# Kernel optimization log

Measured on AMD Instinct MI355X. Metric: run time of the kernel, lower is better.

## Reference

```python
import jax, jax.numpy as jnp
import numpy as np

# Model dims
D_MODEL = 768
N_LAYER = 2
VOCAB = 32000
D_STATE = 16
D_INNER = 2 * D_MODEL          # expand=2
DT_RANK = D_MODEL // 16        # 48
D_CONV = 4
EPS = 1e-5


def rmsnorm(x, w):
    return x * jax.lax.rsqrt(jnp.mean(x * x, axis=-1, keepdims=True) + EPS) * w


def selective_scan(u, delta, A, B, C, D):
    # u: (b,l,di) delta: (b,l,di) A: (di,n) B,C: (b,l,n) D: (di,)
    def step(h, inp):
        delta_t, B_t, C_t, u_t = inp  # (b,di),(b,n),(b,n),(b,di)
        dA = jnp.exp(delta_t[..., None] * A)                      # (b,di,n)
        dBu = delta_t[..., None] * B_t[:, None, :] * u_t[..., None]
        h = dA * h + dBu
        y = jnp.einsum('bdn,bn->bd', h, C_t)
        return h, y

    b = u.shape[0]
    h0 = jnp.zeros((b, D_INNER, D_STATE), dtype=u.dtype)
    xs = (jnp.swapaxes(delta, 0, 1), jnp.swapaxes(B, 0, 1),
          jnp.swapaxes(C, 0, 1), jnp.swapaxes(u, 0, 1))
    _, ys = jax.lax.scan(step, h0, xs)        # ys: (l,b,di)
    y = jnp.swapaxes(ys, 0, 1)
    return y + u * D


def mamba_block(x, in_proj_w, conv_w, conv_b, x_proj_w, dt_proj_w, dt_proj_b,
                A_log, D, out_proj_w):
    b, l, d = x.shape
    xr = x @ in_proj_w.T                       # (b,l,2*di)
    u, res = jnp.split(xr, 2, axis=-1)
    # causal depthwise conv over seq
    uc = jnp.swapaxes(u, 1, 2)                 # (b,di,l)
    uc = jax.lax.conv_general_dilated(
        uc, conv_w[:, None, :], window_strides=(1,),
        padding=[(D_CONV - 1, 0)], feature_group_count=D_INNER,
        dimension_numbers=('NCH', 'OIH', 'NCH'))
    u = jax.nn.silu(jnp.swapaxes(uc + conv_b[None, :, None], 1, 2))
    # ssm
    A = -jnp.exp(A_log)                        # (di,n)
    x_dbl = u @ x_proj_w.T                     # (b,l,dt_rank+2n)
    delta, B, C = jnp.split(x_dbl, [DT_RANK, DT_RANK + D_STATE], axis=-1)
    delta = jax.nn.softplus(delta @ dt_proj_w.T + dt_proj_b)   # (b,l,di)
    y = selective_scan(u, delta, A, B, C, D)
    y = y * jax.nn.silu(res)
    return y @ out_proj_w.T


def setup_inputs() -> dict:
    key = jax.random.key(0)
    ks = jax.random.split(key, 12)
    s = 0.02
    L = N_LAYER
    inp = {
        'input_ids': jax.random.randint(ks[0], (2, 1024), 0, VOCAB),
        'emb': jax.random.normal(ks[1], (VOCAB, D_MODEL), jnp.float32) * s,
        'norm_w': jnp.ones((L, D_MODEL), jnp.float32),
        'in_proj_w': jax.random.normal(ks[2], (L, 2 * D_INNER, D_MODEL), jnp.float32) * s,
        'conv_w': jax.random.normal(ks[3], (L, D_INNER, D_CONV), jnp.float32) * s,
        'conv_b': jnp.zeros((L, D_INNER), jnp.float32),
        'x_proj_w': jax.random.normal(ks[4], (L, DT_RANK + 2 * D_STATE, D_INNER), jnp.float32) * s,
        'dt_proj_w': jax.random.normal(ks[5], (L, D_INNER, DT_RANK), jnp.float32) * s,
        'dt_proj_b': jax.random.normal(ks[6], (L, D_INNER), jnp.float32) * s,
        'A_log': jnp.log(jnp.broadcast_to(jnp.arange(1, D_STATE + 1, dtype=jnp.float32),
                                          (L, D_INNER, D_STATE))),
        'D': jnp.ones((L, D_INNER), jnp.float32),
        'out_proj_w': jax.random.normal(ks[7], (L, D_MODEL, D_INNER), jnp.float32) * s,
        'norm_f_w': jnp.ones((D_MODEL,), jnp.float32),
    }
    return inp


def reference(input_ids, emb, norm_w, in_proj_w, conv_w, conv_b, x_proj_w,
              dt_proj_w, dt_proj_b, A_log, D, out_proj_w, norm_f_w):
    x = emb[input_ids]                         # (b,l,d)
    for i in range(N_LAYER):
        x = x + mamba_block(rmsnorm(x, norm_w[i]), in_proj_w[i], conv_w[i],
                            conv_b[i], x_proj_w[i], dt_proj_w[i], dt_proj_b[i],
                            A_log[i], D[i], out_proj_w[i])
    x = rmsnorm(x, norm_f_w)
    logits = x @ emb.T                         # tied lm_head
    return logits
```

## Files before the change

kernel.cpp:

```cpp
#include <hip/hip_runtime.h>
#include <hip/hip_bf16.h>
#include <cstdint>
#include <cstddef>

#define D_MODEL 768
#define D_INNER 1536
#define DT_RANK 48
#define D_STATE 16
#define SEQ     1024
#define BATCH   2
#define NROWS   2048
#define VOCAB   32000
#define LCHUNK  16
#define NCHUNK  64
#define CHST    49152

typedef __hip_bfloat16 bf16;
typedef short bf16x8 __attribute__((ext_vector_type(8)));
typedef float f32x4  __attribute__((ext_vector_type(4)));
struct bf8 { bf16 v[8]; };

__device__ __forceinline__ void async_copy16(void* lds, const void* gp) {
    __builtin_amdgcn_global_load_lds(
        (const __attribute__((address_space(1))) unsigned int*)gp,
        (__attribute__((address_space(3)))       unsigned int*)lds,
        16, 0, 0);
}


#define LDSP(BUF, AB) (smem + (((BUF)*2 + (AB)) << 15))

#define PHB() do { \
  __builtin_amdgcn_sched_barrier(0); \
  __builtin_amdgcn_s_barrier(); \
  __builtin_amdgcn_sched_barrier(0); \
} while (0)

#define WAIT_VMCNT(n) do { \
  asm volatile("s_waitcnt vmcnt(" #n ")" ::: "memory"); \
  __builtin_amdgcn_sched_barrier(0); \
} while (0)

#define STAGE_A(BUF, H, KT) do { \
  const int ru0_ = (H)*64 + wave*8; \
  const int ru1_ = ru0_ + 128; \
  const bf16* ga0_ = Ag + (size_t)(m0 + ru0_ + (lane >> 3)) * (size_t)K + (size_t)((KT)*64 + swz8); \
  const bf16* ga1_ = Ag + (size_t)(m0 + ru1_ + (lane >> 3)) * (size_t)K + (size_t)((KT)*64 + swz8); \
  async_copy16(LDSP(BUF, 0) + ru0_*128, ga0_); \
  async_copy16(LDSP(BUF, 0) + ru1_*128, ga1_); \
} while (0)

#define STAGE_B(BUF, H, KT) do { \
  const int lb0_ = wave*8, lb1_ = 64 + wave*8; \
  const int rb0_ = ((lb0_ >> 5) << 6) + (H)*32 + (lb0_ & 31); \
  const int rb1_ = ((lb1_ >> 5) << 6) + (H)*32 + (lb1_ & 31); \
  const bf16* gb0_ = Bg + (size_t)(n0 + rb0_ + (lane >> 3)) * (size_t)K + (size_t)((KT)*64 + swz8); \
  const bf16* gb1_ = Bg + (size_t)(n0 + rb1_ + (lane >> 3)) * (size_t)K + (size_t)((KT)*64 + swz8); \
  async_copy16(LDSP(BUF, 1) + rb0_*128, gb0_); \
  async_copy16(LDSP(BUF, 1) + rb1_*128, gb1_); \
} while (0)

#define RDA4(BUF, MH) do { \
  _Pragma("unroll") \
  for (int i2_ = 0; i2_ < 4; ++i2_) { \
    const char* rp_ = LDSP(BUF, 0) + (wr*128 + (MH)*64 + i2_*16 + fm) * 128; \
    a[i2_][0] = *(const bf16x8*)(rp_ + (((kqi    ) ^ fm7) << 4)); \
    a[i2_][1] = *(const bf16x8*)(rp_ + (((4 + kqi) ^ fm7) << 4)); \
  } \
} while (0)

#define RDB4(BUF, NH, DST) do { \
  _Pragma("unroll") \
  for (int j2_ = 0; j2_ < 2; ++j2_) { \
    const char* rp_ = LDSP(BUF, 1) + (wc*64 + (NH)*32 + j2_*16 + fm) * 128; \
    DST[j2_][0] = *(const bf16x8*)(rp_ + (((kqi    ) ^ fm7) << 4)); \
    DST[j2_][1] = *(const bf16x8*)(rp_ + (((4 + kqi) ^ fm7) << 4)); \
  } \
} while (0)

#define QMFMA(MH, NH, BB) do { \
  __builtin_amdgcn_s_setprio(1); \
  _Pragma("unroll") \
  for (int i2_ = 0; i2_ < 4; ++i2_) { \
    _Pragma("unroll") \
    for (int j2_ = 0; j2_ < 2; ++j2_) { \
      acc[(MH)*4 + i2_][(NH)*2 + j2_] = __builtin_amdgcn_mfma_f32_16x16x32_bf16( \
          a[i2_][0], BB[j2_][0], acc[(MH)*4 + i2_][(NH)*2 + j2_], 0, 0, 0); \
      acc[(MH)*4 + i2_][(NH)*2 + j2_] = __builtin_amdgcn_mfma_f32_16x16x32_bf16( \
          a[i2_][1], BB[j2_][1], acc[(MH)*4 + i2_][(NH)*2 + j2_], 0, 0, 0); \
    } \
  } \
  __builtin_amdgcn_s_setprio(0); \
} while (0)

#define ITER(TT, LAST) do { \
  RDA4(0, 0); RDB4(0, 0, b0); \
  STAGE_B(1, 1, (TT) + 1); \
  PHB(); QMFMA(0, 0, b0); PHB(); \
  RDB4(0, 1, b1); \
  if (!(LAST)) STAGE_A(0, 0, (TT) + 2); \
  PHB(); QMFMA(0, 1, b1); PHB(); \
  RDA4(0, 1); \
  if (!(LAST)) STAGE_B(0, 0, (TT) + 2); \
  PHB(); QMFMA(1, 0, b0); PHB(); \
  if (!(LAST)) { STAGE_A(0, 1, (TT) + 2); WAIT_VMCNT(6); } else { WAIT_VMCNT(0); } \
  PHB(); QMFMA(1, 1, b1); PHB(); \
  RDA4(1, 0); RDB4(1, 0, b0); \
  if (!(LAST)) STAGE_B(0, 1, (TT) + 2); \
  PHB(); QMFMA(0, 0, b0); PHB(); \
  RDB4(1, 1, b1); \
  if (!(LAST)) STAGE_A(1, 0, (TT) + 3); \
  PHB(); QMFMA(0, 1, b1); PHB(); \
  RDA4(1, 1); \
  if (!(LAST)) STAGE_B(1, 0, (TT) + 3); \
  PHB(); QMFMA(1, 0, b0); PHB(); \
  if (!(LAST)) { STAGE_A(1, 1, (TT) + 3); WAIT_VMCNT(6); } else { WAIT_VMCNT(0); } \
  PHB(); QMFMA(1, 1, b1); PHB(); \
} while (0)

__global__ __launch_bounds__(512, 2) void gemm256(
    const bf16* __restrict__ Ag, const bf16* __restrict__ Bg,
    float* __restrict__ C, int M, int N, int K, int ntm)
{
    (void)M;
    __shared__ __align__(16) char smem[131072];

    const int cpx  = gridDim.x >> 3;
    const int bid  = blockIdx.x;
    const int wgid = (bid & 7) * cpx + (bid >> 3);
    const int m0 = (wgid % ntm) << 8;
    const int n0 = (wgid / ntm) << 8;

    const int t    = threadIdx.x;
    const int wave = t >> 6, lane = t & 63;
    const int wr = wave >> 2, wc = wave & 3;
    const int fm  = lane & 15, fm7 = lane & 7;
    const int kqi = lane >> 4;
    const int swz8 = (((lane & 7) ^ ((lane >> 3) & 7)) << 3);
    const int nkt = K >> 6;

    f32x4 acc[8][4];
    #pragma unroll
    for (int i = 0; i < 8; ++i)
        #pragma unroll
        for (int j = 0; j < 4; ++j)
            acc[i][j] = {0.f, 0.f, 0.f, 0.f};

    bf16x8 a[4][2], b0[2][2], b1[2][2];

    STAGE_A(0, 0, 0); STAGE_A(0, 1, 0); STAGE_B(0, 0, 0); STAGE_B(0, 1, 0);
    WAIT_VMCNT(4);
    STAGE_A(1, 0, 1); STAGE_A(1, 1, 1); STAGE_B(1, 0, 1);
    WAIT_VMCNT(6);
    PHB();

    int tt = 0;
    #pragma unroll 1
    for (; tt + 2 < nkt; tt += 2) { ITER(tt, false); }
    ITER(tt, true);

    const int lr = (lane >> 4) * 4;
    const int lc = lane & 15;
    #pragma unroll
    for (int i = 0; i < 8; ++i) {
        #pragma unroll
        for (int j = 0; j < 4; ++j) {
            const size_t base = (size_t)(m0 + wr*128 + i*16 + lr) * N
                              + (size_t)(n0 + wc*64 + j*16 + lc);
            #pragma unroll
            for (int r = 0; r < 4; ++r)
                C[base + (size_t)r * N] = acc[i][j][r];
        }
    }
}

template<int EPI>
__global__ __launch_bounds__(256) void gemm_bt(
    const bf16* __restrict__ A, const bf16* __restrict__ B,
    float* __restrict__ C, const float* __restrict__ bias,
    int M, int N, int K, int lda, int ntm)
{
    __shared__ bf16 sA[128 * 32];
    __shared__ bf16 sB[128 * 32];
    const int bid  = blockIdx.x;
    const int m0   = (bid % ntm) * 128;
    const int n0   = (bid / ntm) * 128;
    const int koff = blockIdx.y * K;
    const int t    = threadIdx.x;
    const int wave = t >> 6;
    const int lane = t & 63;
    const int r0 = wave * 16 + (lane >> 2);
    const int c0 = (lane & 3) * 8;
    const int wm = (wave & 1) * 64;
    const int wn = (wave >> 1) * 64;
    const int fm = lane & 15;
    const int kq = (lane >> 4) * 8;

    f32x4 acc[4][4];
    #pragma unroll
    for (int i = 0; i < 4; ++i)
        #pragma unroll
        for (int j = 0; j < 4; ++j)
            acc[i][j] = {0.f, 0.f, 0.f, 0.f};

    int nr0 = n0 + r0;      if (nr0 > N - 1) nr0 = N - 1;
    int nr1 = n0 + 64 + r0; if (nr1 > N - 1) nr1 = N - 1;

    const bf16* gA0 = A + (size_t)(m0 + r0)      * lda + koff + c0;
    const bf16* gA1 = A + (size_t)(m0 + 64 + r0) * lda + koff + c0;
    const bf16* gB0 = B + (size_t)nr0 * lda + koff + c0;
    const bf16* gB1 = B + (size_t)nr1 * lda + koff + c0;
    char* lA0 = (char*)sA + wave * 1024;
    char* lA1 = (char*)sA + 4096 + wave * 1024;
    char* lB0 = (char*)sB + wave * 1024;
    char* lB1 = (char*)sB + 4096 + wave * 1024;

    C += (size_t)blockIdx.y * M * N;

    for (int k0 = 0; k0 < K; k0 += 32) {
        async_copy16(lA0, gA0 + k0);
        async_copy16(lA1, gA1 + k0);
        async_copy16(lB0, gB0 + k0);
        async_copy16(lB1, gB1 + k0);
        __syncthreads();

        bf16x8 af[4], bfr[4];
        #pragma unroll
        for (int i = 0; i < 4; ++i) {
            af[i]  = *(const bf16x8*)&sA[(wm + i * 16 + fm) * 32 + kq];
            bfr[i] = *(const bf16x8*)&sB[(wn + i * 16 + fm) * 32 + kq];
        }
        #pragma unroll
        for (int i = 0; i < 4; ++i)
            #pragma unroll
            for (int j = 0; j < 4; ++j)
                acc[i][j] = __builtin_amdgcn_mfma_f32_16x16x32_bf16(
                    af[i], bfr[j], acc[i][j], 0, 0, 0);
        __syncthreads();
    }

    const int lr = (lane >> 4) * 4;
    const int lc = lane & 15;
    #pragma unroll
    for (int i = 0; i < 4; ++i) {
        #pragma unroll
        for (int j = 0; j < 4; ++j) {
            const int col = n0 + wn + j * 16 + lc;
            if (col >= N) continue;
            #pragma unroll
            for (int r = 0; r < 4; ++r) {
                const int row = m0 + wm + i * 16 + lr + r;
                const size_t o = (size_t)row * N + col;
                float v = acc[i][j][r];
                if (EPI == 1) {
                    C[o] += v;
                } else if (EPI == 2) {
                    v += bias[col];
                    v = (v > 15.f) ? v : __logf(1.f + __expf(v));
                    C[o] = v;
                } else {
                    C[o] = v;
                }
            }
        }
    }
}

__global__ __launch_bounds__(256) void reduce4_kernel(
    const float* __restrict__ p, float* __restrict__ o, int n)
{
    const int i = blockIdx.x * 256 + threadIdx.x;
    if (i >= n) return;
    o[i] = p[i] + p[i + n] + p[i + 2 * n] + p[i + 3 * n];
}

__global__ __launch_bounds__(192) void embed_kernel(
    const int* __restrict__ ids, const float* __restrict__ emb,
    float* __restrict__ x)
{
    const int row = blockIdx.x;
    const int t = threadIdx.x;
    const float4* src = (const float4*)(emb + (size_t)ids[row] * D_MODEL);
    float4* dst = (float4*)(x + (size_t)row * D_MODEL);
    dst[t] = src[t];
}

__global__ __launch_bounds__(256) void rmsnorm_kernel(
    const float* __restrict__ x, const float* __restrict__ w,
    bf16* __restrict__ out)
{
    const int row = blockIdx.x;
    const float* xr = x + (size_t)row * D_MODEL;
    const int t = threadIdx.x;
    float v0 = xr[t], v1 = xr[t + 256], v2 = xr[t + 512];
    float s = v0 * v0 + v1 * v1 + v2 * v2;
    #pragma unroll
    for (int m = 1; m < 64; m <<= 1) s += __shfl_xor(s, m);
    __shared__ float red[4];
    if ((t & 63) == 0) red[t >> 6] = s;
    __syncthreads();
    s = red[0] + red[1] + red[2] + red[3];
    const float sc = rsqrtf(s * (1.f / 768.f) + 1e-5f);
    bf16* o = out + (size_t)row * D_MODEL;
    o[t]       = __float2bfloat16(v0 * sc * w[t]);
    o[t + 256] = __float2bfloat16(v1 * sc * w[t + 256]);
    o[t + 512] = __float2bfloat16(v2 * sc * w[t + 512]);
}

__global__ __launch_bounds__(256) void cvt_bf16_kernel(
    const float* __restrict__ src, bf16* __restrict__ dst, int n)
{
    const int i = (blockIdx.x * 256 + threadIdx.x) * 8;
    if (i >= n) return;
    const float4 a = *(const float4*)(src + i);
    const float4 b = *(const float4*)(src + i + 4);
    bf8 o;
    o.v[0] = __float2bfloat16(a.x); o.v[1] = __float2bfloat16(a.y);
    o.v[2] = __float2bfloat16(a.z); o.v[3] = __float2bfloat16(a.w);
    o.v[4] = __float2bfloat16(b.x); o.v[5] = __float2bfloat16(b.y);
    o.v[6] = __float2bfloat16(b.z); o.v[7] = __float2bfloat16(b.w);
    *(bf8*)(dst + i) = o;
}

__global__ __launch_bounds__(256) void cvt_layer_weights(
    const float* __restrict__ ipw, const float* __restrict__ xpw,
    const float* __restrict__ dtw, const float* __restrict__ opw,
    bf16* __restrict__ wip, bf16* __restrict__ wxp,
    bf16* __restrict__ wdt, bf16* __restrict__ wop)
{
    int i = blockIdx.x * 256 + threadIdx.x;
    if (i < 3072 * 768) { wip[i] = __float2bfloat16(ipw[i]); return; }
    i -= 3072 * 768;
    if (i < 80 * 1536)  { wxp[i] = __float2bfloat16(xpw[i]); return; }
    i -= 80 * 1536;
    if (i < 1536 * 64) {
        const int r = i >> 6, c = i & 63;
        wdt[i] = __float2bfloat16(c < DT_RANK ? dtw[r * DT_RANK + c] : 0.f);
        return;
    }
    i -= 1536 * 64;
    if (i < 768 * 1536) { wop[i] = __float2bfloat16(opw[i]); }
}

__global__ __launch_bounds__(256) void pad_dt_kernel(
    const float* __restrict__ x_dbl, bf16* __restrict__ out)
{
    const int i = blockIdx.x * 256 + threadIdx.x;
    const int r = i >> 6, c = i & 63;
    out[i] = __float2bfloat16(c < DT_RANK ? x_dbl[r * 80 + c] : 0.f);
}

__global__ __launch_bounds__(256) void conv_silu_kernel(
    const float* __restrict__ xr, const float* __restrict__ cw,
    const float* __restrict__ cb, float* __restrict__ uf,
    bf16* __restrict__ ub)
{
    const int idx = blockIdx.x * 256 + threadIdx.x;
    const int di  = idx % D_INNER;
    const int row = idx / D_INNER;
    const int l   = row & (SEQ - 1);
    float acc = cb[di];
    #pragma unroll
    for (int j = 0; j < 4; ++j) {
        const int ll = l - 3 + j;
        if (ll >= 0)
            acc += cw[di * 4 + j] * xr[(size_t)(row - 3 + j) * 3072 + di];
    }
    const float s = acc / (1.f + __expf(-acc));
    uf[idx] = s;
    ub[idx] = __float2bfloat16(s);
}

__global__ __launch_bounds__(256) void scan_pass1(
    const float* __restrict__ delta, const float* __restrict__ u,
    const float* __restrict__ x_dbl, const float* __restrict__ A_log,
    float* __restrict__ P, float* __restrict__ H)
{
    const int n  = threadIdx.x & 15;
    const int g  = threadIdx.x >> 4;
    const int ch = blockIdx.x * 16 + g;
    const int k  = blockIdx.y;
    const int b  = ch / D_INNER;
    const int di = ch % D_INNER;
    const int t0 = k * LCHUNK;

    const float An = -__expf(A_log[di * D_STATE + n]);
    const float* drow = delta + ((size_t)b * SEQ + t0) * D_INNER + di;
    const float* urow = u     + ((size_t)b * SEQ + t0) * D_INNER + di;
    const float* xdr  = x_dbl + ((size_t)b * SEQ + t0) * 80;

    float h = 0.f, ap = 1.f;
    #pragma unroll
    for (int t = 0; t < LCHUNK; ++t) {
        const float dv = drow[t * D_INNER];
        const float uv = urow[t * D_INNER];
        const float Bv = xdr[t * 80 + 48 + n];
        const float a  = __expf(dv * An);
        h = a * h + (dv * Bv) * uv;
        ap *= a;
    }
    const size_t o = (size_t)k * CHST + ch * 16 + n;
    P[o] = ap;
    H[o] = h;
}

__global__ __launch_bounds__(256) void scan_pass2(
    const float* __restrict__ P, const float* __restrict__ H,
    float* __restrict__ Hin)
{
    const int id = blockIdx.x * 256 + threadIdx.x;
    float h = 0.f;
    #pragma unroll 16
    for (int k = 0; k < NCHUNK; ++k) {
        const size_t o = (size_t)k * CHST + id;
        Hin[o] = h;
        h = P[o] * h + H[o];
    }
}

__global__ __launch_bounds__(256) void scan_pass3(
    const float* __restrict__ delta, const float* __restrict__ u,
    const float* __restrict__ x_dbl, const float* __restrict__ xr,
    const float* __restrict__ A_log, const float* __restrict__ Dp,
    const float* __restrict__ Hin, bf16* __restrict__ yb)
{
    const int n  = threadIdx.x & 15;
    const int g  = threadIdx.x >> 4;
    const int ch = blockIdx.x * 16 + g;
    const int k  = blockIdx.y;
    const int b  = ch / D_INNER;
    const int di = ch % D_INNER;
    const int t0 = k * LCHUNK;

    const float An = -__expf(A_log[di * D_STATE + n]);
    const float Dv = Dp[di];
    const float* drow = delta + ((size_t)b * SEQ + t0) * D_INNER + di;
    const float* urow = u     + ((size_t)b * SEQ + t0) * D_INNER + di;
    const float* rrow = xr + ((size_t)b * SEQ + t0) * 3072 + D_INNER + di;
    const float* xdr  = x_dbl + ((size_t)b * SEQ + t0) * 80;
    bf16* yrow = yb + ((size_t)b * SEQ + t0) * D_INNER + di;

    float h = Hin[(size_t)k * CHST + ch * 16 + n];
    #pragma unroll
    for (int t = 0; t < LCHUNK; ++t) {
        const float dv = drow[t * D_INNER];
        const float uv = urow[t * D_INNER];
        const float Bv = xdr[t * 80 + 48 + n];
        const float Cv = xdr[t * 80 + 64 + n];
        const float a  = __expf(dv * An);
        h = a * h + (dv * Bv) * uv;
        float p = h * Cv;
        p += __shfl_xor(p, 1);
        p += __shfl_xor(p, 2);
        p += __shfl_xor(p, 4);
        p += __shfl_xor(p, 8);
        if (n == 0) {
            float y = p + uv * Dv;
            const float r = rrow[t * 3072];
            y *= r / (1.f + __expf(-r));
            yrow[t * D_INNER] = __float2bfloat16(y);
        }
    }
}

extern "C" void kernel_launch(void* const* d_in, const int* in_sizes, int n_in,
                              void* d_out, int out_size, void* d_ws, size_t ws_size,
                              hipStream_t stream)
{
    const int*   ids    = (const int*)  d_in[0];
    const float* emb    = (const float*)d_in[1];
    const float* norm_w = (const float*)d_in[2];
    const float* ipw    = (const float*)d_in[3];
    const float* cw     = (const float*)d_in[4];
    const float* cb     = (const float*)d_in[5];
    const float* xpw    = (const float*)d_in[6];
    const float* dtw    = (const float*)d_in[7];
    const float* dtb    = (const float*)d_in[8];
    const float* alog   = (const float*)d_in[9];
    const float* Dp     = (const float*)d_in[10];
    const float* opw    = (const float*)d_in[11];
    const float* nfw    = (const float*)d_in[12];
    float* out = (float*)d_out;

    char* ws = (char*)d_ws;
    bf16*  emb_bf = (bf16*)ws;  ws += (size_t)VOCAB * D_MODEL * 2;
    float* x      = (float*)ws; ws += (size_t)NROWS * D_MODEL * 4;
    bf16*  xn     = (bf16*)ws;  ws += (size_t)NROWS * D_MODEL * 2;
    bf16*  ub     = (bf16*)ws;  ws += (size_t)NROWS * D_INNER * 2;
    float* xdbl   = (float*)ws; ws += (size_t)NROWS * 80 * 4;
    bf16*  dtraw  = (bf16*)ws;  ws += (size_t)NROWS * 64 * 2;
    bf16*  yb     = (bf16*)ws;  ws += (size_t)NROWS * D_INNER * 2;
    bf16*  wip    = (bf16*)ws;  ws += (size_t)3072 * 768 * 2;
    bf16*  wxp    = (bf16*)ws;  ws += (size_t)80 * 1536 * 2;
    bf16*  wdt    = (bf16*)ws;  ws += (size_t)1536 * 64 * 2;
    bf16*  wop    = (bf16*)ws;  ws += (size_t)768 * 1536 * 2;

    char* ob = (char*)d_out;
    float* xr    = (float*)ob;  ob += (size_t)NROWS * 3072 * 4;
    float* uf    = (float*)ob;  ob += (size_t)NROWS * D_INNER * 4;
    float* delta = (float*)ob;  ob += (size_t)NROWS * D_INNER * 4;
    float* Pbuf  = (float*)ob;  ob += (size_t)NCHUNK * CHST * 4;
    float* Hbuf  = (float*)ob;  ob += (size_t)NCHUNK * CHST * 4;
    float* Hin   = (float*)ob;  ob += (size_t)NCHUNK * CHST * 4;
    float* xpart = (float*)ob;  ob += (size_t)4 * NROWS * 80 * 4;

    cvt_bf16_kernel<<<VOCAB * D_MODEL / 8 / 256, 256, 0, stream>>>(
        emb, emb_bf, VOCAB * D_MODEL);
    embed_kernel<<<NROWS, 192, 0, stream>>>(ids, emb, x);

    for (int l = 0; l < 2; ++l) {
        cvt_layer_weights<<<(3760128 + 255) / 256, 256, 0, stream>>>(
            ipw + (size_t)l * 3072 * 768, xpw + (size_t)l * 80 * 1536,
            dtw + (size_t)l * 1536 * DT_RANK, opw + (size_t)l * 768 * 1536,
            wip, wxp, wdt, wop);
        rmsnorm_kernel<<<NROWS, 256, 0, stream>>>(x, norm_w + l * D_MODEL, xn);
        gemm_bt<0><<<16 * 24, 256, 0, stream>>>(xn, wip, xr, nullptr,
                                                NROWS, 3072, D_MODEL, D_MODEL, 16);
        conv_silu_kernel<<<NROWS * D_INNER / 256, 256, 0, stream>>>(
            xr, cw + (size_t)l * D_INNER * 4, cb + (size_t)l * D_INNER, uf, ub);
        gemm_bt<0><<<dim3(16, 4), 256, 0, stream>>>(ub, wxp, xpart, nullptr,
                                                    NROWS, 80, 384, D_INNER, 16);
        reduce4_kernel<<<(NROWS * 80 + 255) / 256, 256, 0, stream>>>(
            xpart, xdbl, NROWS * 80);
        pad_dt_kernel<<<NROWS * 64 / 256, 256, 0, stream>>>(xdbl, dtraw);
        gemm_bt<2><<<16 * 12, 256, 0, stream>>>(dtraw, wdt, delta,
                                                dtb + (size_t)l * D_INNER,
                                                NROWS, D_INNER, 64, 64, 16);
        scan_pass1<<<dim3(192, NCHUNK), 256, 0, stream>>>(
            delta, uf, xdbl, alog + (size_t)l * D_INNER * D_STATE, Pbuf, Hbuf);
        scan_pass2<<<CHST / 256, 256, 0, stream>>>(Pbuf, Hbuf, Hin);
        scan_pass3<<<dim3(192, NCHUNK), 256, 0, stream>>>(
            delta, uf, xdbl, xr, alog + (size_t)l * D_INNER * D_STATE,
            Dp + (size_t)l * D_INNER, Hin, yb);
        gemm_bt<1><<<16 * 6, 256, 0, stream>>>(yb, wop, x, nullptr,
                                               NROWS, D_MODEL, D_INNER, D_INNER, 16);
    }

    rmsnorm_kernel<<<NROWS, 256, 0, stream>>>(x, nfw, xn);
    gemm256<<<8 * 125, 512, 0, stream>>>(xn, emb_bf, out,
                                         NROWS, VOCAB, D_MODEL, 8);
}
```

Baseline: 971.4 us.

## Fuse reductions with norm, split-K out_proj, batch weight conversion, retune scan chunks

Several changes land together. The scan chunk length goes from 16 to 32, halving the chunk count, and scan_pass2 is fully unrolled. The weight conversion for both layers is done in one launch, and the pad_dt step is folded into the x_proj split-K reduction. The out_proj GEMM now uses split-K into partial buffers, followed by a kernel that reduces the partials, adds the residual and applies the next RMSNorm. The goal is to cut launch count, raise parallelism in the out_proj GEMM and shorten the chunk-carry pass, at the cost of longer sequential per-chunk loops and extra partial-buffer traffic.

```diff
diff --git a/kernel.cpp b/kernel.cpp
--- a/kernel.cpp
+++ b/kernel.cpp
@@ -11,8 +11,8 @@
 #define BATCH   2
 #define NROWS   2048
 #define VOCAB   32000
-#define LCHUNK  16
-#define NCHUNK  64
+#define LCHUNK  32
+#define NCHUNK  32
 #define CHST    49152
 
 typedef __hip_bfloat16 bf16;
@@ -266,12 +266,50 @@
     }
 }
 
-__global__ __launch_bounds__(256) void reduce4_kernel(
-    const float* __restrict__ p, float* __restrict__ o, int n)
+__global__ __launch_bounds__(256) void reduce_xp_kernel(
+    const float* __restrict__ p, float* __restrict__ xdbl,
+    bf16* __restrict__ dtraw)
 {
     const int i = blockIdx.x * 256 + threadIdx.x;
-    if (i >= n) return;
-    o[i] = p[i] + p[i + n] + p[i + 2 * n] + p[i + 3 * n];
+    const float v = p[i] + p[i + 163840] + p[i + 327680] + p[i + 491520];
+    xdbl[i] = v;
+    const int r = i / 80, c = i - r * 80;
+    if (c < 64)
+        dtraw[(r << 6) + c] = __float2bfloat16(c < DT_RANK ? v : 0.f);
+}
+
+__global__ __launch_bounds__(256) void reduce_res_norm_kernel(
+    const float* __restrict__ part, float* __restrict__ x,
+    const float* __restrict__ w, bf16* __restrict__ out)
+{
+    const int row = blockIdx.x;
+    const size_t base = (size_t)row * D_MODEL;
+    const int t = threadIdx.x;
+    float v0, v1, v2;
+    {
+        const int e0 = t, e1 = t + 256, e2 = t + 512;
+        v0 = x[base + e0] + part[base + e0] + part[base + e0 + 1572864]
+           + part[base + e0 + 3145728] + part[base + e0 + 4718592];
+        v1 = x[base + e1] + part[base + e1] + part[base + e1 + 1572864]
+           + part[base + e1 + 3145728] + part[base + e1 + 4718592];
+        v2 = x[base + e2] + part[base + e2] + part[base + e2 + 1572864]
+           + part[base + e2 + 3145728] + part[base + e2 + 4718592];
+    }
+    x[base + t]       = v0;
+    x[base + t + 256] = v1;
+    x[base + t + 512] = v2;
+    float s = v0 * v0 + v1 * v1 + v2 * v2;
+    #pragma unroll
+    for (int m = 1; m < 64; m <<= 1) s += __shfl_xor(s, m);
+    __shared__ float red[4];
+    if ((t & 63) == 0) red[t >> 6] = s;
+    __syncthreads();
+    s = red[0] + red[1] + red[2] + red[3];
+    const float sc = rsqrtf(s * (1.f / 768.f) + 1e-5f);
+    bf16* o = out + base;
+    o[t]       = __float2bfloat16(v0 * sc * w[t]);
+    o[t + 256] = __float2bfloat16(v1 * sc * w[t + 256]);
+    o[t + 512] = __float2bfloat16(v2 * sc * w[t + 512]);
 }
 
 __global__ __launch_bounds__(192) void embed_kernel(
@@ -329,25 +367,26 @@
     bf16* __restrict__ wdt, bf16* __restrict__ wop)
 {
     int i = blockIdx.x * 256 + threadIdx.x;
-    if (i < 3072 * 768) { wip[i] = __float2bfloat16(ipw[i]); return; }
+    const int l = (i >= 3760128) ? 1 : 0;
+    i -= l * 3760128;
+    if (i < 3072 * 768) {
+        wip[l * 3072 * 768 + i] = __float2bfloat16(ipw[l * 3072 * 768 + i]);
+        return;
+    }
     i -= 3072 * 768;
-    if (i < 80 * 1536)  { wxp[i] = __float2bfloat16(xpw[i]); return; }
+    if (i < 80 * 1536) {
+        wxp[l * 80 * 1536 + i] = __float2bfloat16(xpw[l * 80 * 1536 + i]);
+        return;
+    }
     i -= 80 * 1536;
     if (i < 1536 * 64) {
         const int r = i >> 6, c = i & 63;
-        wdt[i] = __float2bfloat16(c < DT_RANK ? dtw[r * DT_RANK + c] : 0.f);
+        wdt[l * 1536 * 64 + i] = __float2bfloat16(
+            c < DT_RANK ? dtw[l * 1536 * DT_RANK + r * DT_RANK + c] : 0.f);
         return;
     }
     i -= 1536 * 64;
-    if (i < 768 * 1536) { wop[i] = __float2bfloat16(opw[i]); }
-}
-
-__global__ __launch_bounds__(256) void pad_dt_kernel(
-    const float* __restrict__ x_dbl, bf16* __restrict__ out)
-{
-    const int i = blockIdx.x * 256 + threadIdx.x;
-    const int r = i >> 6, c = i & 63;
-    out[i] = __float2bfloat16(c < DT_RANK ? x_dbl[r * 80 + c] : 0.f);
+    wop[l * 768 * 1536 + i] = __float2bfloat16(opw[l * 768 * 1536 + i]);
 }
 
 __global__ __launch_bounds__(256) void conv_silu_kernel(
@@ -410,7 +449,7 @@
 {
     const int id = blockIdx.x * 256 + threadIdx.x;
     float h = 0.f;
-    #pragma unroll 16
+    #pragma unroll
     for (int k = 0; k < NCHUNK; ++k) {
         const size_t o = (size_t)k * CHST + id;
         Hin[o] = h;
@@ -490,10 +529,10 @@
     float* xdbl   = (float*)ws; ws += (size_t)NROWS * 80 * 4;
     bf16*  dtraw  = (bf16*)ws;  ws += (size_t)NROWS * 64 * 2;
     bf16*  yb     = (bf16*)ws;  ws += (size_t)NROWS * D_INNER * 2;
-    bf16*  wip    = (bf16*)ws;  ws += (size_t)3072 * 768 * 2;
-    bf16*  wxp    = (bf16*)ws;  ws += (size_t)80 * 1536 * 2;
-    bf16*  wdt    = (bf16*)ws;  ws += (size_t)1536 * 64 * 2;
-    bf16*  wop    = (bf16*)ws;  ws += (size_t)768 * 1536 * 2;
+    bf16*  wip    = (bf16*)ws;  ws += (size_t)2 * 3072 * 768 * 2;
+    bf16*  wxp    = (bf16*)ws;  ws += (size_t)2 * 80 * 1536 * 2;
+    bf16*  wdt    = (bf16*)ws;  ws += (size_t)2 * 1536 * 64 * 2;
+    bf16*  wop    = (bf16*)ws;  ws += (size_t)2 * 768 * 1536 * 2;
 
     char* ob = (char*)d_out;
     float* xr    = (float*)ob;  ob += (size_t)NROWS * 3072 * 4;
@@ -503,40 +542,42 @@
     float* Hbuf  = (float*)ob;  ob += (size_t)NCHUNK * CHST * 4;
     float* Hin   = (float*)ob;  ob += (size_t)NCHUNK * CHST * 4;
     float* xpart = (float*)ob;  ob += (size_t)4 * NROWS * 80 * 4;
+    float* opart = (float*)ob;  ob += (size_t)4 * NROWS * D_MODEL * 4;
 
     cvt_bf16_kernel<<<VOCAB * D_MODEL / 8 / 256, 256, 0, stream>>>(
         emb, emb_bf, VOCAB * D_MODEL);
+    cvt_layer_weights<<<2 * 3760128 / 256, 256, 0, stream>>>(
+        ipw, xpw, dtw, opw, wip, wxp, wdt, wop);
     embed_kernel<<<NROWS, 192, 0, stream>>>(ids, emb, x);
+    rmsnorm_kernel<<<NROWS, 256, 0, stream>>>(x, norm_w, xn);
 
     for (int l = 0; l < 2; ++l) {
-        cvt_layer_weights<<<(3760128 + 255) / 256, 256, 0, stream>>>(
-            ipw + (size_t)l * 3072 * 768, xpw + (size_t)l * 80 * 1536,
-            dtw + (size_t)l * 1536 * DT_RANK, opw + (size_t)l * 768 * 1536,
-            wip, wxp, wdt, wop);
-        rmsnorm_kernel<<<NROWS, 256, 0, stream>>>(x, norm_w + l * D_MODEL, xn);
-        gemm_bt<0><<<16 * 24, 256, 0, stream>>>(xn, wip, xr, nullptr,
-                                                NROWS, 3072, D_MODEL, D_MODEL, 16);
+        gemm_bt<0><<<16 * 24, 256, 0, stream>>>(
+            xn, wip + (size_t)l * 3072 * 768, xr, nullptr,
+            NROWS, 3072, D_MODEL, D_MODEL, 16);
         conv_silu_kernel<<<NROWS * D_INNER / 256, 256, 0, stream>>>(
             xr, cw + (size_t)l * D_INNER * 4, cb + (size_t)l * D_INNER, uf, ub);
-        gemm_bt<0><<<dim3(16, 4), 256, 0, stream>>>(ub, wxp, xpart, nullptr,
-                                                    NROWS, 80, 384, D_INNER, 16);
-        reduce4_kernel<<<(NROWS * 80 + 255) / 256, 256, 0, stream>>>(
-            xpart, xdbl, NROWS * 80);
-        pad_dt_kernel<<<NROWS * 64 / 256, 256, 0, stream>>>(xdbl, dtraw);
-        gemm_bt<2><<<16 * 12, 256, 0, stream>>>(dtraw, wdt, delta,
-                                                dtb + (size_t)l * D_INNER,
-                                                NROWS, D_INNER, 64, 64, 16);
+        gemm_bt<0><<<dim3(16, 4), 256, 0, stream>>>(
+            ub, wxp + (size_t)l * 80 * 1536, xpart, nullptr,
+            NROWS, 80, 384, D_INNER, 16);
+        reduce_xp_kernel<<<NROWS * 80 / 256, 256, 0, stream>>>(
+            xpart, xdbl, dtraw);
+        gemm_bt<2><<<16 * 12, 256, 0, stream>>>(
+            dtraw, wdt + (size_t)l * 1536 * 64, delta,
+            dtb + (size_t)l * D_INNER, NROWS, D_INNER, 64, 64, 16);
         scan_pass1<<<dim3(192, NCHUNK), 256, 0, stream>>>(
             delta, uf, xdbl, alog + (size_t)l * D_INNER * D_STATE, Pbuf, Hbuf);
         scan_pass2<<<CHST / 256, 256, 0, stream>>>(Pbuf, Hbuf, Hin);
         scan_pass3<<<dim3(192, NCHUNK), 256, 0, stream>>>(
             delta, uf, xdbl, xr, alog + (size_t)l * D_INNER * D_STATE,
             Dp + (size_t)l * D_INNER, Hin, yb);
-        gemm_bt<1><<<16 * 6, 256, 0, stream>>>(yb, wop, x, nullptr,
-                                               NROWS, D_MODEL, D_INNER, D_INNER, 16);
-    }
-
-    rmsnorm_kernel<<<NROWS, 256, 0, stream>>>(x, nfw, xn);
+        gemm_bt<0><<<dim3(96, 4), 256, 0, stream>>>(
+            yb, wop + (size_t)l * 768 * 1536, opart, nullptr,
+            NROWS, D_MODEL, 384, D_INNER, 16);
+        reduce_res_norm_kernel<<<NROWS, 256, 0, stream>>>(
+            opart, x, (l == 0) ? (norm_w + D_MODEL) : nfw, xn);
+    }
+
     gemm256<<<8 * 125, 512, 0, stream>>>(xn, emb_bf, out,
                                          NROWS, VOCAB, D_MODEL, 8);
 }
```

Measured after the change: 885.0 us. 1.1x faster.
